# Kernel tuning notes

Measured on AMD Instinct MI355X. Metric: run time of the kernel, lower is better.

Reference implementation:

```python
import jax, jax.numpy as jnp
import numpy as np

ALPHA = 0.2      # LeakyReLU negative slope (hardcoded in StateNetwork: GAT(..., 0.2, 1))
MASK_FILL = 9e-15  # value used for non-edges BEFORE softmax (not -inf, per original code)

N_ENT = 4096     # len(vocab_kge): number of KG entities / GAT nodes
EMB = 64         # embedding_size == gat_emb_size
NHID = 3         # hardcoded in StateNetwork: GAT(gat_emb_size, 3, ...)
BATCH = 4        # number of graphs in graph_rep


def setup_inputs() -> dict:
    key = jax.random.key(0)
    k_adj, k_emb, k_W, k_a, k_fw, k_fb = jax.random.split(key, 6)
    adj = jax.random.randint(k_adj, (BATCH, N_ENT, N_ENT), 0, 2, dtype=jnp.int32)
    ent_emb = jax.random.normal(k_emb, (N_ENT, EMB), dtype=jnp.float32)
    W = jax.random.normal(k_W, (EMB, NHID), dtype=jnp.float32)
    a = jax.random.normal(k_a, (2 * NHID, 1), dtype=jnp.float32)
    fc1_w = jax.random.normal(k_fw, (100, N_ENT * NHID), dtype=jnp.float32) * 0.02
    fc1_b = jax.random.normal(k_fb, (100,), dtype=jnp.float32)
    return {"adj": adj, "ent_emb": ent_emb, "W": W, "a": a, "fc1_w": fc1_w, "fc1_b": fc1_b}


def reference(adj, ent_emb, W, a, fc1_w, fc1_b):
    # GAT layer over the shared entity-embedding node features (same for all graphs).
    h = ent_emb @ W                                   # [N, F]
    F_out = h.shape[1]
    # Pairwise concat score decomposes: e[i,j] = leakyrelu(a1.h_i + a2.h_j)
    src = h @ a[:F_out]                                # [N, 1]
    dst = h @ a[F_out:]                                # [N, 1]
    e = jax.nn.leaky_relu(src + dst.T, negative_slope=ALPHA)   # [N, N]
    # Masked softmax with 9e-15 fill (faithful to torch.where(adj>0, e, 9e-15))
    att = jnp.where(adj > 0, e[None, :, :], jnp.float32(MASK_FILL))  # [B, N, N]
    att = jax.nn.softmax(att, axis=-1)
    h_prime = jnp.einsum('bij,jf->bif', att, h)        # [B, N, F]
    x = jax.nn.elu(h_prime)                            # concat=True -> ELU
    x = x.reshape(adj.shape[0], -1)                    # [B, N*F]
    return x @ fc1_w.T + fc1_b                         # [B, 100]
```

## Files before the change

kernel.cpp:

```cpp
#include <hip/hip_runtime.h>
#include <math.h>

#define N_ENT 4096
#define BATCH 4
#define NHID  3
#define EMB   64
#define ALPHA 0.2f
#define MASK_FILL 9e-15f
#define LOG2E 1.4426950408889634f
#define MASKP (MASK_FILL * LOG2E)

#if defined(__has_builtin)
#  if __has_builtin(__builtin_amdgcn_exp2f)
#    define EXP2F(x) __builtin_amdgcn_exp2f(x)
#  else
#    define EXP2F(x) exp2f(x)
#  endif
#else
#  define EXP2F(x) exp2f(x)
#endif

__global__ __launch_bounds__(256) void prep_kernel(
    const float* __restrict__ emb, const float* __restrict__ W,
    const float* __restrict__ a,
    float* __restrict__ h0G, float* __restrict__ h1G, float* __restrict__ h2G,
    float* __restrict__ dstG, float* __restrict__ srcG)
{
    int j = blockIdx.x * 256 + threadIdx.x;
    if (j >= N_ENT) return;
    const float* er = emb + (size_t)j * EMB;
    float h0 = 0.f, h1 = 0.f, h2 = 0.f;
    #pragma unroll
    for (int e = 0; e < EMB; ++e) {
        float v = er[e];
        h0 += v * W[e * 3 + 0];
        h1 += v * W[e * 3 + 1];
        h2 += v * W[e * 3 + 2];
    }
    h0G[j] = h0; h1G[j] = h1; h2G[j] = h2;
    srcG[j] = (h0 * a[0] + h1 * a[1] + h2 * a[2]) * LOG2E;
    dstG[j] = (h0 * a[3] + h1 * a[4] + h2 * a[5]) * LOG2E;
}

__global__ __launch_bounds__(1024, 8) void gat_row_kernel(
    const int* __restrict__ adj,
    const float* __restrict__ h0G, const float* __restrict__ h1G,
    const float* __restrict__ h2G, const float* __restrict__ dstG,
    const float* __restrict__ srcG, float* __restrict__ xG)
{
    __shared__ float dstL[N_ENT];
    __shared__ float h0L[N_ENT];
    __shared__ float h1L[N_ENT];
    __shared__ float h2L[N_ENT];
    __shared__ float maxdL[16];

    int tid  = threadIdx.x;
    int lane = tid & 63;
    int wid  = tid >> 6;

    float md = -3.4e38f;
    #pragma unroll
    for (int t = tid; t < N_ENT; t += 1024) {
        float dv = dstG[t];
        dstL[t] = dv;
        md = fmaxf(md, dv);
        h0L[t] = h0G[t];
        h1L[t] = h1G[t];
        h2L[t] = h2G[t];
    }
    #pragma unroll
    for (int off = 32; off; off >>= 1) md = fmaxf(md, __shfl_xor(md, off, 64));
    if (lane == 0) maxdL[wid] = md;
    __syncthreads();
    float maxd = maxdL[0];
    #pragma unroll
    for (int t = 1; t < 16; ++t) maxd = fmaxf(maxd, maxdL[t]);

    int gw = blockIdx.x * 16 + wid;

    for (int r = 0; r < 2; ++r) {
        int row = gw * 2 + r;
        int i   = row & (N_ENT - 1);
        float srcp = srcG[i];
        float t0 = srcp + maxd;
        float M  = fmaxf(fmaxf(t0, ALPHA * t0), (float)MASKP);
        float sA = srcp - M;
        float sB = ALPHA * srcp - M;
        float CM = EXP2F((float)MASKP - M);

        const int4* arow = (const int4*)(adj + (size_t)row * N_ENT);

        float l = 0.f, n0 = 0.f, n1 = 0.f, n2 = 0.f;
        #pragma unroll 1
        for (int c = 0; c < 16; ++c) {
            int4 av = arow[c * 64 + lane];
            int jb = (c * 64 + lane) * 4;
            float4 d4 = *(const float4*)&dstL[jb];
            float4 a0 = *(const float4*)&h0L[jb];
            float4 a1 = *(const float4*)&h1L[jb];
            float4 a2 = *(const float4*)&h2L[jb];
            float g0 = EXP2F(fmaxf(sA + d4.x, fmaf(ALPHA, d4.x, sB)));
            float g1 = EXP2F(fmaxf(sA + d4.y, fmaf(ALPHA, d4.y, sB)));
            float g2 = EXP2F(fmaxf(sA + d4.z, fmaf(ALPHA, d4.z, sB)));
            float g3 = EXP2F(fmaxf(sA + d4.w, fmaf(ALPHA, d4.w, sB)));
            float w0 = av.x > 0 ? g0 : CM;
            float w1 = av.y > 0 ? g1 : CM;
            float w2 = av.z > 0 ? g2 : CM;
            float w3 = av.w > 0 ? g3 : CM;
            l  += (w0 + w1) + (w2 + w3);
            n0 = fmaf(w0, a0.x, fmaf(w1, a0.y, fmaf(w2, a0.z, fmaf(w3, a0.w, n0))));
            n1 = fmaf(w0, a1.x, fmaf(w1, a1.y, fmaf(w2, a1.z, fmaf(w3, a1.w, n1))));
            n2 = fmaf(w0, a2.x, fmaf(w1, a2.y, fmaf(w2, a2.z, fmaf(w3, a2.w, n2))));
        }

        #pragma unroll
        for (int off = 32; off; off >>= 1) {
            l  += __shfl_xor(l,  off, 64);
            n0 += __shfl_xor(n0, off, 64);
            n1 += __shfl_xor(n1, off, 64);
            n2 += __shfl_xor(n2, off, 64);
        }

        if (lane == 0) {
            float inv = 1.f / l;
            float hp0 = n0 * inv, hp1 = n1 * inv, hp2 = n2 * inv;
            float* xp = xG + (size_t)row * 3;
            xp[0] = hp0 > 0.f ? hp0 : expm1f(hp0);
            xp[1] = hp1 > 0.f ? hp1 : expm1f(hp1);
            xp[2] = hp2 > 0.f ? hp2 : expm1f(hp2);
        }
    }
}

__global__ __launch_bounds__(256) void fc_kernel(
    const float* __restrict__ xG, const float* __restrict__ w,
    const float* __restrict__ bias, float* __restrict__ out)
{
    int k   = blockIdx.x;
    int tid = threadIdx.x;
    const float4* wr = (const float4*)(w + (size_t)k * (N_ENT * NHID));
    const float4* x0 = (const float4*)(xG + 0 * (N_ENT * NHID));
    const float4* x1 = (const float4*)(xG + 1 * (N_ENT * NHID));
    const float4* x2 = (const float4*)(xG + 2 * (N_ENT * NHID));
    const float4* x3 = (const float4*)(xG + 3 * (N_ENT * NHID));

    float acc0 = 0.f, acc1 = 0.f, acc2 = 0.f, acc3 = 0.f;
    for (int t = tid; t < (N_ENT * NHID / 4); t += 256) {
        float4 wv = wr[t];
        float4 xv;
        xv = x0[t]; acc0 += wv.x*xv.x + wv.y*xv.y + wv.z*xv.z + wv.w*xv.w;
        xv = x1[t]; acc1 += wv.x*xv.x + wv.y*xv.y + wv.z*xv.z + wv.w*xv.w;
        xv = x2[t]; acc2 += wv.x*xv.x + wv.y*xv.y + wv.z*xv.z + wv.w*xv.w;
        xv = x3[t]; acc3 += wv.x*xv.x + wv.y*xv.y + wv.z*xv.z + wv.w*xv.w;
    }

    #pragma unroll
    for (int off = 32; off; off >>= 1) {
        acc0 += __shfl_xor(acc0, off, 64);
        acc1 += __shfl_xor(acc1, off, 64);
        acc2 += __shfl_xor(acc2, off, 64);
        acc3 += __shfl_xor(acc3, off, 64);
    }

    __shared__ float red[4][4];
    int lane = tid & 63, wv_ = tid >> 6;
    if (lane == 0) {
        red[wv_][0] = acc0; red[wv_][1] = acc1;
        red[wv_][2] = acc2; red[wv_][3] = acc3;
    }
    __syncthreads();
    if (tid < 4) {
        float s = red[0][tid] + red[1][tid] + red[2][tid] + red[3][tid] + bias[k];
        out[tid * 100 + k] = s;
    }
}

extern "C" void kernel_launch(void* const* d_in, const int* in_sizes, int n_in,
                              void* d_out, int out_size, void* d_ws, size_t ws_size,
                              hipStream_t stream)
{
    const int*   adj  = (const int*)d_in[0];
    const float* emb  = (const float*)d_in[1];
    const float* W    = (const float*)d_in[2];
    const float* a    = (const float*)d_in[3];
    const float* fc1w = (const float*)d_in[4];
    const float* fc1b = (const float*)d_in[5];
    float* out = (float*)d_out;

    float* ws   = (float*)d_ws;
    float* h0G  = ws;
    float* h1G  = ws + 4096;
    float* h2G  = ws + 8192;
    float* dstG = ws + 12288;
    float* srcG = ws + 16384;
    float* xG   = ws + 20480;

    prep_kernel<<<N_ENT / 256, 256, 0, stream>>>(emb, W, a, h0G, h1G, h2G, dstG, srcG);
    gat_row_kernel<<<512, 1024, 0, stream>>>(adj, h0G, h1G, h2G, dstG, srcG, xG);
    fc_kernel<<<100, 256, 0, stream>>>(xG, fc1w, fc1b, out);
}
```

Baseline: 383.8 us.

## Process two adjacency rows jointly per wave with register double-buffered prefetch

```diff
diff --git a/kernel.cpp b/kernel.cpp
--- a/kernel.cpp
+++ b/kernel.cpp
@@ -42,7 +42,7 @@
     dstG[j] = (h0 * a[3] + h1 * a[4] + h2 * a[5]) * LOG2E;
 }
 
-__global__ __launch_bounds__(1024, 8) void gat_row_kernel(
+__global__ __launch_bounds__(1024, 4) void gat_row_kernel(
     const int* __restrict__ adj,
     const float* __restrict__ h0G, const float* __restrict__ h1G,
     const float* __restrict__ h2G, const float* __restrict__ dstG,
@@ -76,59 +76,100 @@
     #pragma unroll
     for (int t = 1; t < 16; ++t) maxd = fmaxf(maxd, maxdL[t]);
 
-    int gw = blockIdx.x * 16 + wid;
-
-    for (int r = 0; r < 2; ++r) {
-        int row = gw * 2 + r;
-        int i   = row & (N_ENT - 1);
-        float srcp = srcG[i];
-        float t0 = srcp + maxd;
-        float M  = fmaxf(fmaxf(t0, ALPHA * t0), (float)MASKP);
-        float sA = srcp - M;
-        float sB = ALPHA * srcp - M;
-        float CM = EXP2F((float)MASKP - M);
-
-        const int4* arow = (const int4*)(adj + (size_t)row * N_ENT);
-
-        float l = 0.f, n0 = 0.f, n1 = 0.f, n2 = 0.f;
-        #pragma unroll 1
-        for (int c = 0; c < 16; ++c) {
-            int4 av = arow[c * 64 + lane];
-            int jb = (c * 64 + lane) * 4;
-            float4 d4 = *(const float4*)&dstL[jb];
-            float4 a0 = *(const float4*)&h0L[jb];
-            float4 a1 = *(const float4*)&h1L[jb];
-            float4 a2 = *(const float4*)&h2L[jb];
-            float g0 = EXP2F(fmaxf(sA + d4.x, fmaf(ALPHA, d4.x, sB)));
-            float g1 = EXP2F(fmaxf(sA + d4.y, fmaf(ALPHA, d4.y, sB)));
-            float g2 = EXP2F(fmaxf(sA + d4.z, fmaf(ALPHA, d4.z, sB)));
-            float g3 = EXP2F(fmaxf(sA + d4.w, fmaf(ALPHA, d4.w, sB)));
-            float w0 = av.x > 0 ? g0 : CM;
-            float w1 = av.y > 0 ? g1 : CM;
-            float w2 = av.z > 0 ? g2 : CM;
-            float w3 = av.w > 0 ? g3 : CM;
-            l  += (w0 + w1) + (w2 + w3);
-            n0 = fmaf(w0, a0.x, fmaf(w1, a0.y, fmaf(w2, a0.z, fmaf(w3, a0.w, n0))));
-            n1 = fmaf(w0, a1.x, fmaf(w1, a1.y, fmaf(w2, a1.z, fmaf(w3, a1.w, n1))));
-            n2 = fmaf(w0, a2.x, fmaf(w1, a2.y, fmaf(w2, a2.z, fmaf(w3, a2.w, n2))));
+    int gw   = blockIdx.x * 16 + wid;
+    int rowA = gw * 2;
+    int rowB = rowA + 1;
+
+    float srcA = srcG[rowA & (N_ENT - 1)];
+    float srcB = srcG[rowB & (N_ENT - 1)];
+    float tA = srcA + maxd;
+    float MA = fmaxf(fmaxf(tA, ALPHA * tA), (float)MASKP);
+    float sA0 = srcA - MA, sA1 = ALPHA * srcA - MA;
+    float CA  = EXP2F((float)MASKP - MA);
+    float tB = srcB + maxd;
+    float MB = fmaxf(fmaxf(tB, ALPHA * tB), (float)MASKP);
+    float sB0 = srcB - MB, sB1 = ALPHA * srcB - MB;
+    float CB  = EXP2F((float)MASKP - MB);
+
+    const int4* pA = (const int4*)(adj + (size_t)rowA * N_ENT);
+    const int4* pB = (const int4*)(adj + (size_t)rowB * N_ENT);
+
+    int4 c0A = pA[lane],      c0B = pB[lane];
+    int4 c1A = pA[64 + lane], c1B = pB[64 + lane];
+
+    float lA = 0.f, nA0 = 0.f, nA1 = 0.f, nA2 = 0.f;
+    float lB = 0.f, nB0 = 0.f, nB1 = 0.f, nB2 = 0.f;
+
+    #pragma unroll 1
+    for (int c = 0; c < 16; ++c) {
+        int4 avA = c0A, avB = c0B;
+        c0A = c1A; c0B = c1B;
+        int cn = c + 2;
+        if (cn < 16) {
+            c1A = pA[cn * 64 + lane];
+            c1B = pB[cn * 64 + lane];
         }
 
-        #pragma unroll
-        for (int off = 32; off; off >>= 1) {
-            l  += __shfl_xor(l,  off, 64);
-            n0 += __shfl_xor(n0, off, 64);
-            n1 += __shfl_xor(n1, off, 64);
-            n2 += __shfl_xor(n2, off, 64);
+        int jb = (c * 64 + lane) * 4;
+        float4 d4 = *(const float4*)&dstL[jb];
+        float4 a0 = *(const float4*)&h0L[jb];
+        float4 a1 = *(const float4*)&h1L[jb];
+        float4 a2 = *(const float4*)&h2L[jb];
+
+        {
+            float g0 = EXP2F(fmaxf(sA0 + d4.x, fmaf(ALPHA, d4.x, sA1)));
+            float g1 = EXP2F(fmaxf(sA0 + d4.y, fmaf(ALPHA, d4.y, sA1)));
+            float g2 = EXP2F(fmaxf(sA0 + d4.z, fmaf(ALPHA, d4.z, sA1)));
+            float g3 = EXP2F(fmaxf(sA0 + d4.w, fmaf(ALPHA, d4.w, sA1)));
+            float w0 = avA.x > 0 ? g0 : CA;
+            float w1 = avA.y > 0 ? g1 : CA;
+            float w2 = avA.z > 0 ? g2 : CA;
+            float w3 = avA.w > 0 ? g3 : CA;
+            lA += (w0 + w1) + (w2 + w3);
+            nA0 = fmaf(w0, a0.x, fmaf(w1, a0.y, fmaf(w2, a0.z, fmaf(w3, a0.w, nA0))));
+            nA1 = fmaf(w0, a1.x, fmaf(w1, a1.y, fmaf(w2, a1.z, fmaf(w3, a1.w, nA1))));
+            nA2 = fmaf(w0, a2.x, fmaf(w1, a2.y, fmaf(w2, a2.z, fmaf(w3, a2.w, nA2))));
         }
-
-        if (lane == 0) {
-            float inv = 1.f / l;
-            float hp0 = n0 * inv, hp1 = n1 * inv, hp2 = n2 * inv;
-            float* xp = xG + (size_t)row * 3;
-            xp[0] = hp0 > 0.f ? hp0 : expm1f(hp0);
-            xp[1] = hp1 > 0.f ? hp1 : expm1f(hp1);
-            xp[2] = hp2 > 0.f ? hp2 : expm1f(hp2);
+        {
+            float g0 = EXP2F(fmaxf(sB0 + d4.x, fmaf(ALPHA, d4.x, sB1)));
+            float g1 = EXP2F(fmaxf(sB0 + d4.y, fmaf(ALPHA, d4.y, sB1)));
+            float g2 = EXP2F(fmaxf(sB0 + d4.z, fmaf(ALPHA, d4.z, sB1)));
+            float g3 = EXP2F(fmaxf(sB0 + d4.w, fmaf(ALPHA, d4.w, sB1)));
+            float w0 = avB.x > 0 ? g0 : CB;
+            float w1 = avB.y > 0 ? g1 : CB;
+            float w2 = avB.z > 0 ? g2 : CB;
+            float w3 = avB.w > 0 ? g3 : CB;
+            lB += (w0 + w1) + (w2 + w3);
+            nB0 = fmaf(w0, a0.x, fmaf(w1, a0.y, fmaf(w2, a0.z, fmaf(w3, a0.w, nB0))));
+            nB1 = fmaf(w0, a1.x, fmaf(w1, a1.y, fmaf(w2, a1.z, fmaf(w3, a1.w, nB1))));
+            nB2 = fmaf(w0, a2.x, fmaf(w1, a2.y, fmaf(w2, a2.z, fmaf(w3, a2.w, nB2))));
         }
+    }
+
+    #pragma unroll
+    for (int off = 32; off; off >>= 1) {
+        lA  += __shfl_xor(lA,  off, 64);
+        nA0 += __shfl_xor(nA0, off, 64);
+        nA1 += __shfl_xor(nA1, off, 64);
+        nA2 += __shfl_xor(nA2, off, 64);
+        lB  += __shfl_xor(lB,  off, 64);
+        nB0 += __shfl_xor(nB0, off, 64);
+        nB1 += __shfl_xor(nB1, off, 64);
+        nB2 += __shfl_xor(nB2, off, 64);
+    }
+
+    if (lane == 0) {
+        float* xp = xG + (size_t)rowA * 3;
+        float invA = 1.f / lA;
+        float h0 = nA0 * invA, h1 = nA1 * invA, h2 = nA2 * invA;
+        xp[0] = h0 > 0.f ? h0 : expm1f(h0);
+        xp[1] = h1 > 0.f ? h1 : expm1f(h1);
+        xp[2] = h2 > 0.f ? h2 : expm1f(h2);
+        float invB = 1.f / lB;
+        float g0 = nB0 * invB, g1 = nB1 * invB, g2 = nB2 * invB;
+        xp[3] = g0 > 0.f ? g0 : expm1f(g0);
+        xp[4] = g1 > 0.f ? g1 : expm1f(g1);
+        xp[5] = g2 > 0.f ? g2 : expm1f(g2);
     }
 }
 
```

Result: no change. 383.1 us (-0.2%).

## Process all four batch graphs per row to share exp work and prefetch adjacency

Applied to the files above, without the earlier changes.

```diff
diff --git a/kernel.cpp b/kernel.cpp
--- a/kernel.cpp
+++ b/kernel.cpp
@@ -42,7 +42,7 @@
     dstG[j] = (h0 * a[3] + h1 * a[4] + h2 * a[5]) * LOG2E;
 }
 
-__global__ __launch_bounds__(1024, 8) void gat_row_kernel(
+__global__ __launch_bounds__(1024, 4) void gat_row_kernel(
     const int* __restrict__ adj,
     const float* __restrict__ h0G, const float* __restrict__ h1G,
     const float* __restrict__ h2G, const float* __restrict__ dstG,
@@ -76,59 +76,125 @@
     #pragma unroll
     for (int t = 1; t < 16; ++t) maxd = fmaxf(maxd, maxdL[t]);
 
-    int gw = blockIdx.x * 16 + wid;
-
-    for (int r = 0; r < 2; ++r) {
-        int row = gw * 2 + r;
-        int i   = row & (N_ENT - 1);
-        float srcp = srcG[i];
-        float t0 = srcp + maxd;
-        float M  = fmaxf(fmaxf(t0, ALPHA * t0), (float)MASKP);
-        float sA = srcp - M;
-        float sB = ALPHA * srcp - M;
-        float CM = EXP2F((float)MASKP - M);
-
-        const int4* arow = (const int4*)(adj + (size_t)row * N_ENT);
-
-        float l = 0.f, n0 = 0.f, n1 = 0.f, n2 = 0.f;
-        #pragma unroll 1
-        for (int c = 0; c < 16; ++c) {
-            int4 av = arow[c * 64 + lane];
-            int jb = (c * 64 + lane) * 4;
-            float4 d4 = *(const float4*)&dstL[jb];
-            float4 a0 = *(const float4*)&h0L[jb];
-            float4 a1 = *(const float4*)&h1L[jb];
-            float4 a2 = *(const float4*)&h2L[jb];
-            float g0 = EXP2F(fmaxf(sA + d4.x, fmaf(ALPHA, d4.x, sB)));
-            float g1 = EXP2F(fmaxf(sA + d4.y, fmaf(ALPHA, d4.y, sB)));
-            float g2 = EXP2F(fmaxf(sA + d4.z, fmaf(ALPHA, d4.z, sB)));
-            float g3 = EXP2F(fmaxf(sA + d4.w, fmaf(ALPHA, d4.w, sB)));
-            float w0 = av.x > 0 ? g0 : CM;
-            float w1 = av.y > 0 ? g1 : CM;
-            float w2 = av.z > 0 ? g2 : CM;
-            float w3 = av.w > 0 ? g3 : CM;
-            l  += (w0 + w1) + (w2 + w3);
-            n0 = fmaf(w0, a0.x, fmaf(w1, a0.y, fmaf(w2, a0.z, fmaf(w3, a0.w, n0))));
-            n1 = fmaf(w0, a1.x, fmaf(w1, a1.y, fmaf(w2, a1.z, fmaf(w3, a1.w, n1))));
-            n2 = fmaf(w0, a2.x, fmaf(w1, a2.y, fmaf(w2, a2.z, fmaf(w3, a2.w, n2))));
-        }
-
-        #pragma unroll
-        for (int off = 32; off; off >>= 1) {
-            l  += __shfl_xor(l,  off, 64);
-            n0 += __shfl_xor(n0, off, 64);
-            n1 += __shfl_xor(n1, off, 64);
-            n2 += __shfl_xor(n2, off, 64);
-        }
-
-        if (lane == 0) {
-            float inv = 1.f / l;
-            float hp0 = n0 * inv, hp1 = n1 * inv, hp2 = n2 * inv;
-            float* xp = xG + (size_t)row * 3;
-            xp[0] = hp0 > 0.f ? hp0 : expm1f(hp0);
-            xp[1] = hp1 > 0.f ? hp1 : expm1f(hp1);
-            xp[2] = hp2 > 0.f ? hp2 : expm1f(hp2);
-        }
+    int i = blockIdx.x * 16 + wid;
+
+    float srcp = srcG[i];
+    float tt = srcp + maxd;
+    float M  = fmaxf(fmaxf(tt, ALPHA * tt), (float)MASKP);
+    float s0 = srcp - M, s1 = ALPHA * srcp - M;
+    float C  = EXP2F((float)MASKP - M);
+
+    const int4* p0 = (const int4*)(adj + ((size_t)0 * N_ENT + i) * N_ENT);
+    const int4* p1 = (const int4*)(adj + ((size_t)1 * N_ENT + i) * N_ENT);
+    const int4* p2 = (const int4*)(adj + ((size_t)2 * N_ENT + i) * N_ENT);
+    const int4* p3 = (const int4*)(adj + ((size_t)3 * N_ENT + i) * N_ENT);
+
+    int4 cur0 = p0[lane],      cur1 = p1[lane],      cur2 = p2[lane],      cur3 = p3[lane];
+    int4 nxt0 = p0[64 + lane], nxt1 = p1[64 + lane], nxt2 = p2[64 + lane], nxt3 = p3[64 + lane];
+
+    float l0 = 0.f, n00 = 0.f, n01 = 0.f, n02 = 0.f;
+    float l1 = 0.f, n10 = 0.f, n11 = 0.f, n12 = 0.f;
+    float l2 = 0.f, n20 = 0.f, n21 = 0.f, n22 = 0.f;
+    float l3 = 0.f, n30 = 0.f, n31 = 0.f, n32 = 0.f;
+
+    #pragma unroll 1
+    for (int c = 0; c < 16; ++c) {
+        int4 a0v = cur0, a1v = cur1, a2v = cur2, a3v = cur3;
+        cur0 = nxt0; cur1 = nxt1; cur2 = nxt2; cur3 = nxt3;
+        int cn = (c + 2) & 15;
+        nxt0 = p0[cn * 64 + lane];
+        nxt1 = p1[cn * 64 + lane];
+        nxt2 = p2[cn * 64 + lane];
+        nxt3 = p3[cn * 64 + lane];
+
+        int jb = (c * 64 + lane) * 4;
+        float4 d4 = *(const float4*)&dstL[jb];
+        float4 h0 = *(const float4*)&h0L[jb];
+        float4 h1 = *(const float4*)&h1L[jb];
+        float4 h2 = *(const float4*)&h2L[jb];
+
+        float g0 = EXP2F(fmaxf(s0 + d4.x, fmaf(ALPHA, d4.x, s1)));
+        float g1 = EXP2F(fmaxf(s0 + d4.y, fmaf(ALPHA, d4.y, s1)));
+        float g2 = EXP2F(fmaxf(s0 + d4.z, fmaf(ALPHA, d4.z, s1)));
+        float g3 = EXP2F(fmaxf(s0 + d4.w, fmaf(ALPHA, d4.w, s1)));
+
+        {
+            float w0 = a0v.x > 0 ? g0 : C, w1 = a0v.y > 0 ? g1 : C;
+            float w2 = a0v.z > 0 ? g2 : C, w3 = a0v.w > 0 ? g3 : C;
+            l0 += (w0 + w1) + (w2 + w3);
+            n00 = fmaf(w0, h0.x, fmaf(w1, h0.y, fmaf(w2, h0.z, fmaf(w3, h0.w, n00))));
+            n01 = fmaf(w0, h1.x, fmaf(w1, h1.y, fmaf(w2, h1.z, fmaf(w3, h1.w, n01))));
+            n02 = fmaf(w0, h2.x, fmaf(w1, h2.y, fmaf(w2, h2.z, fmaf(w3, h2.w, n02))));
+        }
+        {
+            float w0 = a1v.x > 0 ? g0 : C, w1 = a1v.y > 0 ? g1 : C;
+            float w2 = a1v.z > 0 ? g2 : C, w3 = a1v.w > 0 ? g3 : C;
+            l1 += (w0 + w1) + (w2 + w3);
+            n10 = fmaf(w0, h0.x, fmaf(w1, h0.y, fmaf(w2, h0.z, fmaf(w3, h0.w, n10))));
+            n11 = fmaf(w0, h1.x, fmaf(w1, h1.y, fmaf(w2, h1.z, fmaf(w3, h1.w, n11))));
+            n12 = fmaf(w0, h2.x, fmaf(w1, h2.y, fmaf(w2, h2.z, fmaf(w3, h2.w, n12))));
+        }
+        {
+            float w0 = a2v.x > 0 ? g0 : C, w1 = a2v.y > 0 ? g1 : C;
+            float w2 = a2v.z > 0 ? g2 : C, w3 = a2v.w > 0 ? g3 : C;
+            l2 += (w0 + w1) + (w2 + w3);
+            n20 = fmaf(w0, h0.x, fmaf(w1, h0.y, fmaf(w2, h0.z, fmaf(w3, h0.w, n20))));
+            n21 = fmaf(w0, h1.x, fmaf(w1, h1.y, fmaf(w2, h1.z, fmaf(w3, h1.w, n21))));
+            n22 = fmaf(w0, h2.x, fmaf(w1, h2.y, fmaf(w2, h2.z, fmaf(w3, h2.w, n22))));
+        }
+        {
+            float w0 = a3v.x > 0 ? g0 : C, w1 = a3v.y > 0 ? g1 : C;
+            float w2 = a3v.z > 0 ? g2 : C, w3 = a3v.w > 0 ? g3 : C;
+            l3 += (w0 + w1) + (w2 + w3);
+            n30 = fmaf(w0, h0.x, fmaf(w1, h0.y, fmaf(w2, h0.z, fmaf(w3, h0.w, n30))));
+            n31 = fmaf(w0, h1.x, fmaf(w1, h1.y, fmaf(w2, h1.z, fmaf(w3, h1.w, n31))));
+            n32 = fmaf(w0, h2.x, fmaf(w1, h2.y, fmaf(w2, h2.z, fmaf(w3, h2.w, n32))));
+        }
+    }
+
+    #pragma unroll
+    for (int off = 32; off; off >>= 1) {
+        l0  += __shfl_xor(l0,  off, 64);
+        n00 += __shfl_xor(n00, off, 64);
+        n01 += __shfl_xor(n01, off, 64);
+        n02 += __shfl_xor(n02, off, 64);
+        l1  += __shfl_xor(l1,  off, 64);
+        n10 += __shfl_xor(n10, off, 64);
+        n11 += __shfl_xor(n11, off, 64);
+        n12 += __shfl_xor(n12, off, 64);
+        l2  += __shfl_xor(l2,  off, 64);
+        n20 += __shfl_xor(n20, off, 64);
+        n21 += __shfl_xor(n21, off, 64);
+        n22 += __shfl_xor(n22, off, 64);
+        l3  += __shfl_xor(l3,  off, 64);
+        n30 += __shfl_xor(n30, off, 64);
+        n31 += __shfl_xor(n31, off, 64);
+        n32 += __shfl_xor(n32, off, 64);
+    }
+
+    if (lane == 0) {
+        float inv, v0, v1, v2;
+        float* xp;
+        inv = 1.f / l0; v0 = n00*inv; v1 = n01*inv; v2 = n02*inv;
+        xp = xG + ((size_t)0 * N_ENT + i) * 3;
+        xp[0] = v0 > 0.f ? v0 : expm1f(v0);
+        xp[1] = v1 > 0.f ? v1 : expm1f(v1);
+        xp[2] = v2 > 0.f ? v2 : expm1f(v2);
+        inv = 1.f / l1; v0 = n10*inv; v1 = n11*inv; v2 = n12*inv;
+        xp = xG + ((size_t)1 * N_ENT + i) * 3;
+        xp[0] = v0 > 0.f ? v0 : expm1f(v0);
+        xp[1] = v1 > 0.f ? v1 : expm1f(v1);
+        xp[2] = v2 > 0.f ? v2 : expm1f(v2);
+        inv = 1.f / l2; v0 = n20*inv; v1 = n21*inv; v2 = n22*inv;
+        xp = xG + ((size_t)2 * N_ENT + i) * 3;
+        xp[0] = v0 > 0.f ? v0 : expm1f(v0);
+        xp[1] = v1 > 0.f ? v1 : expm1f(v1);
+        xp[2] = v2 > 0.f ? v2 : expm1f(v2);
+        inv = 1.f / l3; v0 = n30*inv; v1 = n31*inv; v2 = n32*inv;
+        xp = xG + ((size_t)3 * N_ENT + i) * 3;
+        xp[0] = v0 > 0.f ? v0 : expm1f(v0);
+        xp[1] = v1 > 0.f ? v1 : expm1f(v1);
+        xp[2] = v2 > 0.f ? v2 : expm1f(v2);
     }
 }
 
@@ -196,6 +262,6 @@
     float* xG   = ws + 20480;
 
     prep_kernel<<<N_ENT / 256, 256, 0, stream>>>(emb, W, a, h0G, h1G, h2G, dstG, srcG);
-    gat_row_kernel<<<512, 1024, 0, stream>>>(adj, h0G, h1G, h2G, dstG, srcG, xG);
+    gat_row_kernel<<<N_ENT / 16, 1024, 0, stream>>>(adj, h0G, h1G, h2G, dstG, srcG, xG);
     fc_kernel<<<100, 256, 0, stream>>>(xG, fc1w, fc1b, out);
 }
```

Result: no change. 384.2 us (+0.1%).
